# Performance work log

Hardware: AMD Instinct MI355X
Metric: run time of the kernel (lower is better)

The kernel has to match this reference:

```python
import jax, jax.numpy as jnp
import numpy as np

B, A, T, NH, NEMB = 8, 32, 64, 256, 256
E = A * (A - 1)  # fully-connected directed edges, no self-loops


def _onehot_edges():
    # NRI-style: rows of off-diagonal pairs (send i -> recv j, i != j)
    send_idx, recv_idx = [], []
    for i in range(A):
        for j in range(A):
            if i != j:
                send_idx.append(i)
                recv_idx.append(j)
    rel_send = jax.nn.one_hot(jnp.array(send_idx), A, dtype=jnp.float32)
    rel_rec = jax.nn.one_hot(jnp.array(recv_idx), A, dtype=jnp.float32)
    return rel_rec, rel_send


def setup_inputs() -> dict:
    key = jax.random.key(0)
    k1, k2, k3 = jax.random.split(key, 3)
    h = jax.random.normal(k1, (B, A, T, NH), dtype=jnp.float32)
    rel_rec, rel_send = _onehot_edges()
    # nn.Linear(2*n_h, n_emb): W [n_emb, 2*n_h], b [n_emb]
    lim = 1.0 / np.sqrt(2 * NH)
    W = jax.random.uniform(k2, (NEMB, 2 * NH), minval=-lim, maxval=lim, dtype=jnp.float32)
    b = jax.random.uniform(k3, (NEMB,), minval=-lim, maxval=lim, dtype=jnp.float32)
    return {"h": h, "rel_rec": rel_rec, "rel_send": rel_send, "W": W, "b": b}


def reference(h, rel_rec, rel_send, W, b):
    # h: [B, A, T, NH]; rel_rec/rel_send: [E, A] one-hot selectors
    # Equivalent to reshape->batched matmul->reshape in the torch code,
    # expressed as a single contraction over atoms.
    receivers = jnp.einsum('ea,bath->beth', rel_rec, h)   # [B, E, T, NH]
    senders = jnp.einsum('ea,bath->beth', rel_send, h)    # [B, E, T, NH]
    edges = jnp.concatenate([senders, receivers], axis=-1)  # [B, E, T, 2*NH]
    return jnp.einsum('betf,of->beto', edges, W) + b        # [B, E, T, NEMB]
```

## Files before the change

kernel.cpp:

```cpp
#include <hip/hip_runtime.h>
#include <hip/hip_bf16.h>

using f32x4  = __attribute__((ext_vector_type(4))) float;
using bf16x8 = __attribute__((ext_vector_type(8))) short;
using s16x4  = __attribute__((ext_vector_type(4))) short;

constexpr int kB  = 8;
constexpr int kA  = 32;
constexpr int kT  = 64;
constexpr int kNH = 256;
constexpr int kNE = 256;
constexpr int kE  = kA * (kA - 1);
constexpr int kM  = kB * kA * kT;
constexpr int kK  = kNH;
constexpr int kN  = 2 * kNE;

__device__ __forceinline__ unsigned short rne_bf16(float f) {
    unsigned int u = __float_as_uint(f);
    u += 0x7fffu + ((u >> 16) & 1u);
    return (unsigned short)(u >> 16);
}
__device__ __forceinline__ float bf16_f32(unsigned short h) {
    return __uint_as_float(((unsigned int)h) << 16);
}
__device__ __forceinline__ void split2(float x, unsigned short& h, unsigned short& m) {
    h = rne_bf16(x);
    float r1 = x - bf16_f32(h);
    m = rne_bf16(r1);
}

__global__ __launch_bounds__(256) void k_split_all(const float* __restrict__ hsrc,
                                                   unsigned short* __restrict__ a1,
                                                   unsigned short* __restrict__ a2,
                                                   const float* __restrict__ W,
                                                   unsigned short* __restrict__ b1,
                                                   unsigned short* __restrict__ b2,
                                                   const float* __restrict__ rel_rec,
                                                   const float* __restrict__ rel_send,
                                                   int* __restrict__ ij2e) {
    const int bidx = blockIdx.x;
    if (bidx < 4096) {
        int idx = bidx * 256 + threadIdx.x;
        f32x4 v = ((const f32x4*)hsrc)[idx];
        s16x4 o1, o2;
#pragma unroll
        for (int j = 0; j < 4; ++j) {
            unsigned short h, m;
            split2(v[j], h, m);
            o1[j] = (short)h; o2[j] = (short)m;
        }
        *(s16x4*)(a1 + (size_t)idx * 4) = o1;
        *(s16x4*)(a2 + (size_t)idx * 4) = o2;
        return;
    }
    const int wb  = bidx - 4096;
    int idx = wb * 256 + threadIdx.x;
    int n  = idx >> 6;
    int k4 = (idx & 63) << 2;
    const float* s = (n < kNE) ? (W + (size_t)n * (2 * kNH) + k4)
                               : (W + (size_t)(n - kNE) * (2 * kNH) + kNH + k4);
    f32x4 v = *(const f32x4*)s;
    s16x4 o1, o2;
#pragma unroll
    for (int j = 0; j < 4; ++j) {
        unsigned short h, m;
        split2(v[j], h, m);
        o1[j] = (short)h; o2[j] = (short)m;
    }
    size_t off = (size_t)n * kK + k4;
    *(s16x4*)(b1 + off) = o1;
    *(s16x4*)(b2 + off) = o2;

    if (wb < 4) {
        int e = wb * 256 + threadIdx.x;
        if (e < kE) {
            int ir = 0, is = 0;
            for (int a = 0; a < kA; ++a) {
                if (rel_rec[(size_t)e * kA + a]  > 0.5f) ir = a;
                if (rel_send[(size_t)e * kA + a] > 0.5f) is = a;
            }
            ij2e[is * kA + ir] = e;
        }
    }
}

#define GLL(g, l) __builtin_amdgcn_global_load_lds( \
    (const __attribute__((address_space(1))) void*)(g), \
    (__attribute__((address_space(3))) void*)(l), 16, 0, 0)

__global__ __launch_bounds__(256) void k_gemm4(const unsigned short* __restrict__ Ah,
                                               const unsigned short* __restrict__ Am,
                                               const unsigned short* __restrict__ Bh,
                                               const unsigned short* __restrict__ Bm,
                                               float* __restrict__ P) {
    __shared__ unsigned short sAh[128 * 32], sAm[128 * 32];
    __shared__ unsigned short sBh[128 * 32], sBm[128 * 32];
    const int tid  = threadIdx.x;
    const int lane = tid & 63;
    const int wave = tid >> 6;
    const int wr = wave >> 1, wc = wave & 1;
    const int bid = blockIdx.x;
    const int xcd = bid & 7;
    const int idx = bid >> 3;
    const int bn  = idx & 3;
    const int bm  = xcd * 16 + (idx >> 2);

    const int sr   = tid >> 2;
    const int scb  = (tid & 3) << 4;
    const int scbs = scb ^ (((sr >> 1) & 3) << 4);
    const size_t rA  = (size_t)(bm * 128 + sr) * kK + (scbs >> 1);
    const size_t rB  = (size_t)(bn * 128 + sr) * kK + (scbs >> 1);
    const size_t rA1 = rA + (size_t)64 * kK;
    const size_t rB1 = rB + (size_t)64 * kK;
    const int l0 = tid * 8, l1 = 64 * 32 + tid * 8;

    const int fr  = lane & 15;
    const int fkb = (lane >> 4) << 4;
    const int swz = ((fr >> 1) & 3) << 4;

    f32x4 acc[4][4] = {};

    for (int kt = 0; kt < kK / 32; ++kt) {
        const int kk = kt * 32;
        __syncthreads();
        GLL(Ah + rA + kk, sAh + l0);  GLL(Ah + rA1 + kk, sAh + l1);
        GLL(Am + rA + kk, sAm + l0);  GLL(Am + rA1 + kk, sAm + l1);
        GLL(Bh + rB + kk, sBh + l0);  GLL(Bh + rB1 + kk, sBh + l1);
        GLL(Bm + rB + kk, sBm + l0);  GLL(Bm + rB1 + kk, sBm + l1);
        __syncthreads();

        bf16x8 ah[4], am[4], bh[4], bmf[4];
#pragma unroll
        for (int mi = 0; mi < 4; ++mi) {
            int row = wr * 64 + mi * 16 + fr;
            int off = row * 64 + (fkb ^ swz);
            ah[mi] = *(const bf16x8*)((const char*)sAh + off);
            am[mi] = *(const bf16x8*)((const char*)sAm + off);
        }
#pragma unroll
        for (int ni = 0; ni < 4; ++ni) {
            int row = wc * 64 + ni * 16 + fr;
            int off = row * 64 + (fkb ^ swz);
            bh[ni]  = *(const bf16x8*)((const char*)sBh + off);
            bmf[ni] = *(const bf16x8*)((const char*)sBm + off);
        }
#pragma unroll
        for (int mi = 0; mi < 4; ++mi)
#pragma unroll
            for (int ni = 0; ni < 4; ++ni) {
                f32x4 c = acc[mi][ni];
                c = __builtin_amdgcn_mfma_f32_16x16x32_bf16(ah[mi], bh[ni],  c, 0, 0, 0);
                c = __builtin_amdgcn_mfma_f32_16x16x32_bf16(ah[mi], bmf[ni], c, 0, 0, 0);
                c = __builtin_amdgcn_mfma_f32_16x16x32_bf16(am[mi], bh[ni],  c, 0, 0, 0);
                c = __builtin_amdgcn_mfma_f32_16x16x32_bf16(am[mi], bmf[ni], c, 0, 0, 0);
                acc[mi][ni] = c;
            }
    }

    const int col = lane & 15;
    const int rb  = (lane >> 4) << 2;
#pragma unroll
    for (int mi = 0; mi < 4; ++mi)
#pragma unroll
        for (int ni = 0; ni < 4; ++ni) {
            int n = bn * 128 + wc * 64 + ni * 16 + col;
#pragma unroll
            for (int r = 0; r < 4; ++r) {
                int m = bm * 128 + wr * 64 + mi * 16 + rb + r;
                P[(size_t)m * kN + n] = acc[mi][ni][r];
            }
        }
}

__global__ __launch_bounds__(256) void k_gather2(const float* __restrict__ P,
                                                 const float* __restrict__ bias,
                                                 const int* __restrict__ ij2e,
                                                 float* __restrict__ out) {
    const int bid = blockIdx.x;
    const int b  = bid & 7;
    const int th = (bid >> 3) & 1;
    const int gi = (bid >> 4) & 7;
    const int gj = bid >> 7;
    __shared__ int se[16];
    if (threadIdx.x < 16) {
        int si = threadIdx.x >> 2, rj = threadIdx.x & 3;
        int i = gi * 4 + si, j = gj * 4 + rj;
        se[threadIdx.x] = (i == j) ? -1 : ij2e[i * kA + j];
    }
    __syncthreads();
    int e[16];
#pragma unroll
    for (int k = 0; k < 16; ++k) e[k] = se[k];

    const int c  = threadIdx.x & 63;
    const int t0 = th * 32 + (threadIdx.x >> 6);
    f32x4 bv = ((const f32x4*)bias)[c];
    const float* Pb = P + (size_t)(b * kA) * kT * kN;
    float* outb = out + (size_t)b * kE * kT * kNE;

    for (int t = t0; t < th * 32 + 32; t += 4) {
        f32x4 ps[4], pr[4];
#pragma unroll
        for (int si = 0; si < 4; ++si)
            ps[si] = *(const f32x4*)(Pb + ((size_t)(gi * 4 + si) * kT + t) * kN + c * 4);
#pragma unroll
        for (int rj = 0; rj < 4; ++rj)
            pr[rj] = *(const f32x4*)(Pb + ((size_t)(gj * 4 + rj) * kT + t) * kN + kNE + c * 4);
#pragma unroll
        for (int si = 0; si < 4; ++si)
#pragma unroll
            for (int rj = 0; rj < 4; ++rj) {
                int ee = e[si * 4 + rj];
                if (ee >= 0) {
                    f32x4 v = ps[si] + pr[rj] + bv;
                    __builtin_nontemporal_store(
                        v, (f32x4*)(outb + ((size_t)ee * kT + t) * kNE + c * 4));
                }
            }
    }
}

extern "C" void kernel_launch(void* const* d_in, const int* in_sizes, int n_in,
                              void* d_out, int out_size, void* d_ws, size_t ws_size,
                              hipStream_t stream) {
    const float* h    = (const float*)d_in[0];
    const float* rrec = (const float*)d_in[1];
    const float* rsnd = (const float*)d_in[2];
    const float* W    = (const float*)d_in[3];
    const float* bias = (const float*)d_in[4];
    float* out = (float*)d_out;

    char* ws = (char*)d_ws;
    const size_t MB = 1024 * 1024;
    unsigned short* Ah = (unsigned short*)(ws);
    unsigned short* Am = (unsigned short*)(ws + 8 * MB);
    unsigned short* Bh = (unsigned short*)(ws + 16 * MB);
    unsigned short* Bm = (unsigned short*)(ws + 16 * MB + 256 * 1024);
    float* P   = (float*)(ws + 17 * MB);
    int* ij2e  = (int*)(ws + 49 * MB);

    k_split_all<<<dim3(4096 + 128), dim3(256), 0, stream>>>(h, Ah, Am,
                                                            W, Bh, Bm,
                                                            rrec, rsnd, ij2e);
    k_gemm4    <<<dim3(512),        dim3(256), 0, stream>>>(Ah, Am, Bh, Bm, P);
    k_gather2  <<<dim3(1024),       dim3(256), 0, stream>>>(P, bias, ij2e, out);
}
```

Before: 129.1 us.

## Double-buffer LDS tiles in split-bf16 GEMM and drop low-low MFMA term

The GEMM kernel now keeps two LDS buffers per operand and issues global-to-LDS loads for the next K tile while MFMAs run on the current one, with one barrier per iteration instead of two. It also removes the Am*Bm product from the three-way bf16 split emulation of fp32, cutting MFMA work by a quarter. The LDS footprint doubles to 64 KB, which may limit occupancy. Dropping the low-low term slightly reduces accuracy. The loop also has no explicit wait on the async loads before the barrier, so correctness depends on the barrier draining them.

```diff
diff --git a/kernel.cpp b/kernel.cpp
--- a/kernel.cpp
+++ b/kernel.cpp
@@ -88,13 +88,13 @@
     (const __attribute__((address_space(1))) void*)(g), \
     (__attribute__((address_space(3))) void*)(l), 16, 0, 0)
 
-__global__ __launch_bounds__(256) void k_gemm4(const unsigned short* __restrict__ Ah,
+__global__ __launch_bounds__(256) void k_gemm5(const unsigned short* __restrict__ Ah,
                                                const unsigned short* __restrict__ Am,
                                                const unsigned short* __restrict__ Bh,
                                                const unsigned short* __restrict__ Bm,
                                                float* __restrict__ P) {
-    __shared__ unsigned short sAh[128 * 32], sAm[128 * 32];
-    __shared__ unsigned short sBh[128 * 32], sBm[128 * 32];
+    __shared__ unsigned short sAh[2][128 * 32], sAm[2][128 * 32];
+    __shared__ unsigned short sBh[2][128 * 32], sBm[2][128 * 32];
     const int tid  = threadIdx.x;
     const int lane = tid & 63;
     const int wave = tid >> 6;
@@ -120,29 +120,36 @@
 
     f32x4 acc[4][4] = {};
 
-    for (int kt = 0; kt < kK / 32; ++kt) {
-        const int kk = kt * 32;
-        __syncthreads();
-        GLL(Ah + rA + kk, sAh + l0);  GLL(Ah + rA1 + kk, sAh + l1);
-        GLL(Am + rA + kk, sAm + l0);  GLL(Am + rA1 + kk, sAm + l1);
-        GLL(Bh + rB + kk, sBh + l0);  GLL(Bh + rB1 + kk, sBh + l1);
-        GLL(Bm + rB + kk, sBm + l0);  GLL(Bm + rB1 + kk, sBm + l1);
-        __syncthreads();
+#define STAGE(buf, kk)                                                        \
+    do {                                                                      \
+        GLL(Ah + rA + (kk), sAh[buf] + l0);  GLL(Ah + rA1 + (kk), sAh[buf] + l1); \
+        GLL(Am + rA + (kk), sAm[buf] + l0);  GLL(Am + rA1 + (kk), sAm[buf] + l1); \
+        GLL(Bh + rB + (kk), sBh[buf] + l0);  GLL(Bh + rB1 + (kk), sBh[buf] + l1); \
+        GLL(Bm + rB + (kk), sBm[buf] + l0);  GLL(Bm + rB1 + (kk), sBm[buf] + l1); \
+    } while (0)
+
+    STAGE(0, 0);
+    __syncthreads();
+
+#pragma unroll
+    for (int kt = 0; kt < 8; ++kt) {
+        const int cur = kt & 1;
+        if (kt < 7) STAGE(cur ^ 1, (kt + 1) * 32);
 
         bf16x8 ah[4], am[4], bh[4], bmf[4];
 #pragma unroll
         for (int mi = 0; mi < 4; ++mi) {
             int row = wr * 64 + mi * 16 + fr;
             int off = row * 64 + (fkb ^ swz);
-            ah[mi] = *(const bf16x8*)((const char*)sAh + off);
-            am[mi] = *(const bf16x8*)((const char*)sAm + off);
+            ah[mi] = *(const bf16x8*)((const char*)sAh[cur] + off);
+            am[mi] = *(const bf16x8*)((const char*)sAm[cur] + off);
         }
 #pragma unroll
         for (int ni = 0; ni < 4; ++ni) {
             int row = wc * 64 + ni * 16 + fr;
             int off = row * 64 + (fkb ^ swz);
-            bh[ni]  = *(const bf16x8*)((const char*)sBh + off);
-            bmf[ni] = *(const bf16x8*)((const char*)sBm + off);
+            bh[ni]  = *(const bf16x8*)((const char*)sBh[cur] + off);
+            bmf[ni] = *(const bf16x8*)((const char*)sBm[cur] + off);
         }
 #pragma unroll
         for (int mi = 0; mi < 4; ++mi)
@@ -152,10 +159,11 @@
                 c = __builtin_amdgcn_mfma_f32_16x16x32_bf16(ah[mi], bh[ni],  c, 0, 0, 0);
                 c = __builtin_amdgcn_mfma_f32_16x16x32_bf16(ah[mi], bmf[ni], c, 0, 0, 0);
                 c = __builtin_amdgcn_mfma_f32_16x16x32_bf16(am[mi], bh[ni],  c, 0, 0, 0);
-                c = __builtin_amdgcn_mfma_f32_16x16x32_bf16(am[mi], bmf[ni], c, 0, 0, 0);
                 acc[mi][ni] = c;
             }
-    }
+        __syncthreads();
+    }
+#undef STAGE
 
     const int col = lane & 15;
     const int rb  = (lane >> 4) << 2;
@@ -242,6 +250,6 @@
     k_split_all<<<dim3(4096 + 128), dim3(256), 0, stream>>>(h, Ah, Am,
                                                             W, Bh, Bm,
                                                             rrec, rsnd, ij2e);
-    k_gemm4    <<<dim3(512),        dim3(256), 0, stream>>>(Ah, Am, Bh, Bm, P);
+    k_gemm5    <<<dim3(512),        dim3(256), 0, stream>>>(Ah, Am, Bh, Bm, P);
     k_gather2  <<<dim3(1024),       dim3(256), 0, stream>>>(P, bias, ij2e, out);
 }
```

After: 128.4 us. About the same (-0.5%).

## Fuse split, GEMM and gather into one persistent kernel with flag sync

Applied to the files above, without the earlier changes.

Merges the three kernels into a single 512-block kernel. Each block splits its slice of h and W, then runs its GEMM tile, then performs a gather phase, with global atomic flags providing the dependencies between phases. This removes two kernel launch gaps and lets phases overlap across blocks. It also drops the lo*lo MFMA term, cutting GEMM compute by a quarter at a small precision cost. The spin-wait approach relies on all 512 blocks being co-resident (launch_bounds 256,2) to avoid deadlock, and it adds a memset to reset the flags.

```diff
diff --git a/kernel.cpp b/kernel.cpp
--- a/kernel.cpp
+++ b/kernel.cpp
@@ -15,6 +15,11 @@
 constexpr int kK  = kNH;
 constexpr int kN  = 2 * kNE;
 
+constexpr int FW = 0;
+constexpr int FL = 1;
+constexpr int FA = 2;
+constexpr int FP = 130;
+
 __device__ __forceinline__ unsigned short rne_bf16(float f) {
     unsigned int u = __float_as_uint(f);
     u += 0x7fffu + ((u >> 16) & 1u);
@@ -29,194 +34,212 @@
     m = rne_bf16(r1);
 }
 
-__global__ __launch_bounds__(256) void k_split_all(const float* __restrict__ hsrc,
-                                                   unsigned short* __restrict__ a1,
-                                                   unsigned short* __restrict__ a2,
-                                                   const float* __restrict__ W,
-                                                   unsigned short* __restrict__ b1,
-                                                   unsigned short* __restrict__ b2,
-                                                   const float* __restrict__ rel_rec,
-                                                   const float* __restrict__ rel_send,
-                                                   int* __restrict__ ij2e) {
-    const int bidx = blockIdx.x;
-    if (bidx < 4096) {
-        int idx = bidx * 256 + threadIdx.x;
-        f32x4 v = ((const f32x4*)hsrc)[idx];
-        s16x4 o1, o2;
-#pragma unroll
-        for (int j = 0; j < 4; ++j) {
-            unsigned short h, m;
-            split2(v[j], h, m);
-            o1[j] = (short)h; o2[j] = (short)m;
-        }
-        *(s16x4*)(a1 + (size_t)idx * 4) = o1;
-        *(s16x4*)(a2 + (size_t)idx * 4) = o2;
-        return;
-    }
-    const int wb  = bidx - 4096;
-    int idx = wb * 256 + threadIdx.x;
-    int n  = idx >> 6;
-    int k4 = (idx & 63) << 2;
-    const float* s = (n < kNE) ? (W + (size_t)n * (2 * kNH) + k4)
-                               : (W + (size_t)(n - kNE) * (2 * kNH) + kNH + k4);
-    f32x4 v = *(const f32x4*)s;
-    s16x4 o1, o2;
-#pragma unroll
-    for (int j = 0; j < 4; ++j) {
-        unsigned short h, m;
-        split2(v[j], h, m);
-        o1[j] = (short)h; o2[j] = (short)m;
-    }
-    size_t off = (size_t)n * kK + k4;
-    *(s16x4*)(b1 + off) = o1;
-    *(s16x4*)(b2 + off) = o2;
-
-    if (wb < 4) {
-        int e = wb * 256 + threadIdx.x;
-        if (e < kE) {
-            int ir = 0, is = 0;
-            for (int a = 0; a < kA; ++a) {
-                if (rel_rec[(size_t)e * kA + a]  > 0.5f) ir = a;
-                if (rel_send[(size_t)e * kA + a] > 0.5f) is = a;
-            }
-            ij2e[is * kA + ir] = e;
-        }
-    }
-}
-
 #define GLL(g, l) __builtin_amdgcn_global_load_lds( \
     (const __attribute__((address_space(1))) void*)(g), \
     (__attribute__((address_space(3))) void*)(l), 16, 0, 0)
 
-__global__ __launch_bounds__(256) void k_gemm4(const unsigned short* __restrict__ Ah,
-                                               const unsigned short* __restrict__ Am,
-                                               const unsigned short* __restrict__ Bh,
-                                               const unsigned short* __restrict__ Bm,
-                                               float* __restrict__ P) {
+#define FLAG_ADD(i) __hip_atomic_fetch_add(&flags[i], 1u, __ATOMIC_RELEASE, \
+                                           __HIP_MEMORY_SCOPE_AGENT)
+#define FLAG_WAIT(i, tgt)                                                        \
+    while (__hip_atomic_load(&flags[i], __ATOMIC_ACQUIRE,                        \
+                             __HIP_MEMORY_SCOPE_AGENT) < (unsigned)(tgt))        \
+        __builtin_amdgcn_s_sleep(2)
+
+__global__ __launch_bounds__(256, 2) void k_all(const float* __restrict__ hsrc,
+                                                const float* __restrict__ W,
+                                                const float* __restrict__ rel_rec,
+                                                const float* __restrict__ rel_send,
+                                                const float* __restrict__ bias,
+                                                unsigned short* __restrict__ a1,
+                                                unsigned short* __restrict__ a2,
+                                                unsigned short* __restrict__ b1,
+                                                unsigned short* __restrict__ b2,
+                                                float* __restrict__ P,
+                                                int* __restrict__ ij2e,
+                                                unsigned int* flags,
+                                                float* __restrict__ out) {
     __shared__ unsigned short sAh[128 * 32], sAm[128 * 32];
     __shared__ unsigned short sBh[128 * 32], sBm[128 * 32];
-    const int tid  = threadIdx.x;
-    const int lane = tid & 63;
-    const int wave = tid >> 6;
-    const int wr = wave >> 1, wc = wave & 1;
+
     const int bid = blockIdx.x;
+    const int tid = threadIdx.x;
     const int xcd = bid & 7;
     const int idx = bid >> 3;
     const int bn  = idx & 3;
     const int bm  = xcd * 16 + (idx >> 2);
 
-    const int sr   = tid >> 2;
-    const int scb  = (tid & 3) << 4;
-    const int scbs = scb ^ (((sr >> 1) & 3) << 4);
-    const size_t rA  = (size_t)(bm * 128 + sr) * kK + (scbs >> 1);
-    const size_t rB  = (size_t)(bn * 128 + sr) * kK + (scbs >> 1);
-    const size_t rA1 = rA + (size_t)64 * kK;
-    const size_t rB1 = rB + (size_t)64 * kK;
-    const int l0 = tid * 8, l1 = 64 * 32 + tid * 8;
-
-    const int fr  = lane & 15;
-    const int fkb = (lane >> 4) << 4;
-    const int swz = ((fr >> 1) & 3) << 4;
-
-    f32x4 acc[4][4] = {};
-
-    for (int kt = 0; kt < kK / 32; ++kt) {
-        const int kk = kt * 32;
-        __syncthreads();
-        GLL(Ah + rA + kk, sAh + l0);  GLL(Ah + rA1 + kk, sAh + l1);
-        GLL(Am + rA + kk, sAm + l0);  GLL(Am + rA1 + kk, sAm + l1);
-        GLL(Bh + rB + kk, sBh + l0);  GLL(Bh + rB1 + kk, sBh + l1);
-        GLL(Bm + rB + kk, sBm + l0);  GLL(Bm + rB1 + kk, sBm + l1);
-        __syncthreads();
-
-        bf16x8 ah[4], am[4], bh[4], bmf[4];
-#pragma unroll
-        for (int mi = 0; mi < 4; ++mi) {
-            int row = wr * 64 + mi * 16 + fr;
-            int off = row * 64 + (fkb ^ swz);
-            ah[mi] = *(const bf16x8*)((const char*)sAh + off);
-            am[mi] = *(const bf16x8*)((const char*)sAm + off);
-        }
-#pragma unroll
-        for (int ni = 0; ni < 4; ++ni) {
-            int row = wc * 64 + ni * 16 + fr;
-            int off = row * 64 + (fkb ^ swz);
-            bh[ni]  = *(const bf16x8*)((const char*)sBh + off);
-            bmf[ni] = *(const bf16x8*)((const char*)sBm + off);
-        }
+    {
+        const int row0 = bm * 128 + bn * 32;
+        const size_t base4 = (size_t)row0 * 64;
+#pragma unroll
+        for (int r = 0; r < 8; ++r) {
+            size_t i4 = base4 + (size_t)r * 256 + tid;
+            f32x4 v = ((const f32x4*)hsrc)[i4];
+            s16x4 o1, o2;
+#pragma unroll
+            for (int j = 0; j < 4; ++j) {
+                unsigned short h, m;
+                split2(v[j], h, m);
+                o1[j] = (short)h; o2[j] = (short)m;
+            }
+            *(s16x4*)(a1 + i4 * 4) = o1;
+            *(s16x4*)(a2 + i4 * 4) = o2;
+        }
+        float wv = (bid < kNE) ? W[(size_t)bid * (2 * kNH) + tid]
+                               : W[(size_t)(bid - kNE) * (2 * kNH) + kNH + tid];
+        unsigned short wh, wm;
+        split2(wv, wh, wm);
+        b1[(size_t)bid * kK + tid] = wh;
+        b2[(size_t)bid * kK + tid] = wm;
+        if (bid < 4) {
+            int e = bid * 256 + tid;
+            if (e < kE) {
+                int ir = 0, is = 0;
+                for (int a = 0; a < kA; ++a) {
+                    if (rel_rec[(size_t)e * kA + a]  > 0.5f) ir = a;
+                    if (rel_send[(size_t)e * kA + a] > 0.5f) is = a;
+                }
+                ij2e[is * kA + ir] = e;
+            }
+        }
+        __threadfence();
+        __syncthreads();
+        if (tid == 0) {
+            FLAG_ADD(FA + bm);
+            FLAG_ADD(FW);
+            if (bid < 4) FLAG_ADD(FL);
+        }
+    }
+
+    {
+        if (tid == 0) { FLAG_WAIT(FA + bm, 4); FLAG_WAIT(FW, 512); }
+        __syncthreads();
+
+        const int lane = tid & 63;
+        const int wave = tid >> 6;
+        const int wr = wave >> 1, wc = wave & 1;
+
+        const int sr   = tid >> 2;
+        const int scb  = (tid & 3) << 4;
+        const int scbs = scb ^ (((sr >> 1) & 3) << 4);
+        const size_t rA  = (size_t)(bm * 128 + sr) * kK + (scbs >> 1);
+        const size_t rB  = (size_t)(bn * 128 + sr) * kK + (scbs >> 1);
+        const size_t rA1 = rA + (size_t)64 * kK;
+        const size_t rB1 = rB + (size_t)64 * kK;
+        const int l0 = tid * 8, l1 = 64 * 32 + tid * 8;
+
+        const int fr  = lane & 15;
+        const int fkb = (lane >> 4) << 4;
+        const int swz = ((fr >> 1) & 3) << 4;
+
+        f32x4 acc[4][4] = {};
+
+#pragma unroll
+        for (int kt = 0; kt < 8; ++kt) {
+            const int kk = kt * 32;
+            __syncthreads();
+            GLL(a1 + rA + kk, sAh + l0);  GLL(a1 + rA1 + kk, sAh + l1);
+            GLL(a2 + rA + kk, sAm + l0);  GLL(a2 + rA1 + kk, sAm + l1);
+            GLL(b1 + rB + kk, sBh + l0);  GLL(b1 + rB1 + kk, sBh + l1);
+            GLL(b2 + rB + kk, sBm + l0);  GLL(b2 + rB1 + kk, sBm + l1);
+            __syncthreads();
+
+            bf16x8 ah[4], am[4], bh[4], bmf[4];
+#pragma unroll
+            for (int mi = 0; mi < 4; ++mi) {
+                int row = wr * 64 + mi * 16 + fr;
+                int off = row * 64 + (fkb ^ swz);
+                ah[mi] = *(const bf16x8*)((const char*)sAh + off);
+                am[mi] = *(const bf16x8*)((const char*)sAm + off);
+            }
+#pragma unroll
+            for (int ni = 0; ni < 4; ++ni) {
+                int row = wc * 64 + ni * 16 + fr;
+                int off = row * 64 + (fkb ^ swz);
+                bh[ni]  = *(const bf16x8*)((const char*)sBh + off);
+                bmf[ni] = *(const bf16x8*)((const char*)sBm + off);
+            }
+#pragma unroll
+            for (int mi = 0; mi < 4; ++mi)
+#pragma unroll
+                for (int ni = 0; ni < 4; ++ni) {
+                    f32x4 c = acc[mi][ni];
+                    c = __builtin_amdgcn_mfma_f32_16x16x32_bf16(ah[mi], bh[ni],  c, 0, 0, 0);
+                    c = __builtin_amdgcn_mfma_f32_16x16x32_bf16(ah[mi], bmf[ni], c, 0, 0, 0);
+                    c = __builtin_amdgcn_mfma_f32_16x16x32_bf16(am[mi], bh[ni],  c, 0, 0, 0);
+                    acc[mi][ni] = c;
+                }
+        }
+
+        const int col = lane & 15;
+        const int rb  = (lane >> 4) << 2;
 #pragma unroll
         for (int mi = 0; mi < 4; ++mi)
 #pragma unroll
             for (int ni = 0; ni < 4; ++ni) {
-                f32x4 c = acc[mi][ni];
-                c = __builtin_amdgcn_mfma_f32_16x16x32_bf16(ah[mi], bh[ni],  c, 0, 0, 0);
-                c = __builtin_amdgcn_mfma_f32_16x16x32_bf16(ah[mi], bmf[ni], c, 0, 0, 0);
-                c = __builtin_amdgcn_mfma_f32_16x16x32_bf16(am[mi], bh[ni],  c, 0, 0, 0);
-                c = __builtin_amdgcn_mfma_f32_16x16x32_bf16(am[mi], bmf[ni], c, 0, 0, 0);
-                acc[mi][ni] = c;
-            }
+                int n = bn * 128 + wc * 64 + ni * 16 + col;
+#pragma unroll
+                for (int r = 0; r < 4; ++r) {
+                    int m = bm * 128 + wr * 64 + mi * 16 + rb + r;
+                    P[(size_t)m * kN + n] = acc[mi][ni][r];
+                }
+            }
+        __threadfence();
+        __syncthreads();
+        if (tid == 0) FLAG_ADD(FP + bm);
     }
 
-    const int col = lane & 15;
-    const int rb  = (lane >> 4) << 2;
-#pragma unroll
-    for (int mi = 0; mi < 4; ++mi)
-#pragma unroll
-        for (int ni = 0; ni < 4; ++ni) {
-            int n = bn * 128 + wc * 64 + ni * 16 + col;
-#pragma unroll
-            for (int r = 0; r < 4; ++r) {
-                int m = bm * 128 + wr * 64 + mi * 16 + rb + r;
-                P[(size_t)m * kN + n] = acc[mi][ni][r];
-            }
-        }
-}
-
-__global__ __launch_bounds__(256) void k_gather2(const float* __restrict__ P,
-                                                 const float* __restrict__ bias,
-                                                 const int* __restrict__ ij2e,
-                                                 float* __restrict__ out) {
-    const int bid = blockIdx.x;
-    const int b  = bid & 7;
-    const int th = (bid >> 3) & 1;
-    const int gi = (bid >> 4) & 7;
-    const int gj = bid >> 7;
-    __shared__ int se[16];
-    if (threadIdx.x < 16) {
-        int si = threadIdx.x >> 2, rj = threadIdx.x & 3;
-        int i = gi * 4 + si, j = gj * 4 + rj;
-        se[threadIdx.x] = (i == j) ? -1 : ij2e[i * kA + j];
-    }
-    __syncthreads();
-    int e[16];
-#pragma unroll
-    for (int k = 0; k < 16; ++k) e[k] = se[k];
-
-    const int c  = threadIdx.x & 63;
-    const int t0 = th * 32 + (threadIdx.x >> 6);
-    f32x4 bv = ((const f32x4*)bias)[c];
-    const float* Pb = P + (size_t)(b * kA) * kT * kN;
-    float* outb = out + (size_t)b * kE * kT * kNE;
-
-    for (int t = t0; t < th * 32 + 32; t += 4) {
-        f32x4 ps[4], pr[4];
-#pragma unroll
-        for (int si = 0; si < 4; ++si)
-            ps[si] = *(const f32x4*)(Pb + ((size_t)(gi * 4 + si) * kT + t) * kN + c * 4);
-#pragma unroll
-        for (int rj = 0; rj < 4; ++rj)
-            pr[rj] = *(const f32x4*)(Pb + ((size_t)(gj * 4 + rj) * kT + t) * kN + kNE + c * 4);
-#pragma unroll
-        for (int si = 0; si < 4; ++si)
-#pragma unroll
-            for (int rj = 0; rj < 4; ++rj) {
-                int ee = e[si * 4 + rj];
-                if (ee >= 0) {
-                    f32x4 v = ps[si] + pr[rj] + bv;
-                    __builtin_nontemporal_store(
-                        v, (f32x4*)(outb + ((size_t)ee * kT + t) * kNE + c * 4));
-                }
-            }
+    {
+        const int b  = bid & 7;
+        const int gi = (bid >> 3) & 7;
+        const int gj = (bid >> 6) & 7;
+        const int m0 = b * 16 + 2 * gi;
+        const int m2 = b * 16 + 2 * gj;
+        if (tid == 0) {
+            FLAG_WAIT(FL, 4);
+            FLAG_WAIT(FP + m0, 4);  FLAG_WAIT(FP + m0 + 1, 4);
+            FLAG_WAIT(FP + m2, 4);  FLAG_WAIT(FP + m2 + 1, 4);
+        }
+        __syncthreads();
+
+        int* se = (int*)sAh;
+        if (tid < 16) {
+            int si = tid >> 2, rj = tid & 3;
+            int i = gi * 4 + si, j = gj * 4 + rj;
+            se[tid] = (i == j) ? -1 : ij2e[i * kA + j];
+        }
+        __syncthreads();
+        int e[16];
+#pragma unroll
+        for (int k = 0; k < 16; ++k) e[k] = se[k];
+
+        const int c = tid & 63;
+        const int w = tid >> 6;
+        f32x4 bv = ((const f32x4*)bias)[c];
+        const float* Pb = P + (size_t)(b * kA) * kT * kN;
+        float* outb = out + (size_t)b * kE * kT * kNE;
+
+        for (int i = 0; i < 16; ++i) {
+            int t = w + i * 4;
+            f32x4 ps[4], pr[4];
+#pragma unroll
+            for (int si = 0; si < 4; ++si)
+                ps[si] = *(const f32x4*)(Pb + ((size_t)(gi * 4 + si) * kT + t) * kN + c * 4);
+#pragma unroll
+            for (int rj = 0; rj < 4; ++rj)
+                pr[rj] = *(const f32x4*)(Pb + ((size_t)(gj * 4 + rj) * kT + t) * kN + kNE + c * 4);
+#pragma unroll
+            for (int si = 0; si < 4; ++si)
+#pragma unroll
+                for (int rj = 0; rj < 4; ++rj) {
+                    int ee = e[si * 4 + rj];
+                    if (ee >= 0) {
+                        f32x4 v = ps[si] + pr[rj] + bv;
+                        __builtin_nontemporal_store(
+                            v, (f32x4*)(outb + ((size_t)ee * kT + t) * kNE + c * 4));
+                    }
+                }
+        }
     }
 }
 
@@ -238,10 +261,9 @@
     unsigned short* Bm = (unsigned short*)(ws + 16 * MB + 256 * 1024);
     float* P   = (float*)(ws + 17 * MB);
     int* ij2e  = (int*)(ws + 49 * MB);
-
-    k_split_all<<<dim3(4096 + 128), dim3(256), 0, stream>>>(h, Ah, Am,
-                                                            W, Bh, Bm,
-                                                            rrec, rsnd, ij2e);
-    k_gemm4    <<<dim3(512),        dim3(256), 0, stream>>>(Ah, Am, Bh, Bm, P);
-    k_gather2  <<<dim3(1024),       dim3(256), 0, stream>>>(P, bias, ij2e, out);
-}
+    unsigned int* flags = (unsigned int*)(ws + 49 * MB + 4096);
+
+    hipMemsetAsync(flags, 0, 4096, stream);
+    k_all<<<dim3(512), dim3(256), 0, stream>>>(h, W, rrec, rsnd, bias,
+                                               Ah, Am, Bh, Bm, P, ij2e, flags, out);
+}
```

Measured after the change: 317.9 us. 146% more time.
